# Kernel optimization log

Measured on AMD Instinct MI355X. Metric: run time of the kernel, lower is better.

The kernel has to match this reference:

```python
import jax, jax.numpy as jnp
import numpy as np

B, F, V, D = 16384, 26, 100000, 64
H1, H2 = 512, 256
IN_DIM = F * D + F * (F - 1) // 2  # 1664 + 325 = 1989
# upper-triangle (i<j) pair indices in row-major order == itertools.combinations order
IU, JU = np.triu_indices(F, k=1)


def setup_inputs() -> dict:
    key = jax.random.key(0)
    ks = jax.random.split(key, 9)
    idx = jax.random.randint(ks[0], (B, F), 0, V)
    tables = jax.random.normal(ks[1], (F, V, D), dtype=jnp.float32) * 0.01
    W1 = jax.random.normal(ks[2], (IN_DIM, H1), dtype=jnp.float32) * (IN_DIM ** -0.5)
    b1 = jnp.zeros((H1,), jnp.float32)
    W2 = jax.random.normal(ks[3], (H1, H2), dtype=jnp.float32) * (H1 ** -0.5)
    b2 = jnp.zeros((H2,), jnp.float32)
    W3 = jax.random.normal(ks[4], (H2, 1), dtype=jnp.float32) * (H2 ** -0.5)
    b3 = jnp.zeros((1,), jnp.float32)
    return {"idx": idx, "tables": tables, "W1": W1, "b1": b1,
            "W2": W2, "b2": b2, "W3": W3, "b3": b3}


def reference(idx, tables, W1, b1, W2, b2, W3, b3):
    # embedding lookup: tables[f, idx[b, f]] -> [B, F, D]
    emb = tables[jnp.arange(F)[None, :], idx]
    # fused dot-interaction: batched Gram matrix + triangular gather
    gram = jnp.einsum('bfd,bgd->bfg', emb, emb)  # [B, F, F]
    inter = gram[:, IU, JU]                      # [B, F*(F-1)/2]
    joint = jnp.concatenate([emb.reshape(B, F * D), inter], axis=1)
    h = jax.nn.relu(joint @ W1 + b1)
    h = jax.nn.relu(h @ W2 + b2)
    return (h @ W3 + b3).squeeze(-1)  # [B] logits
```

## Files before the change

kernel.cpp:

```cpp
#include <hip/hip_runtime.h>

#define B_SZ   16384
#define F_N    26
#define V_N    100000
#define D_N    64
#define H1_N   512
#define H2_N   256
#define IN_DIM 1989
#define KPAD   2048

typedef _Float16 half8_t __attribute__((ext_vector_type(8)));
typedef _Float16 half4_t __attribute__((ext_vector_type(4)));
typedef float    floatx4 __attribute__((ext_vector_type(4)));

#define MFMA16(a, b, c) __builtin_amdgcn_mfma_f32_16x16x32_f16((a), (b), (c), 0, 0, 0)

__device__ __forceinline__ void load_lds16(const void* g, void* l) {
    __builtin_amdgcn_global_load_lds(
        (const __attribute__((address_space(1))) unsigned int*)g,
        (__attribute__((address_space(3))) unsigned int*)l,
        16, 0, 0);
}

__global__ __launch_bounds__(256) void prep_w(const float* __restrict__ W,
                                              _Float16* __restrict__ WT,
                                              int K, int N, int Kpad) {
    int t = blockIdx.x * 256 + threadIdx.x;
    if (t >= N * Kpad) return;
    int k = t / N;
    int n = t - k * N;
    WT[(size_t)n * Kpad + k] = (k < K) ? (_Float16)W[(size_t)k * N + n] : (_Float16)0.f;
}

#define EMB_STRIDE 72
#define EMB_PER_SAMPLE (32 * EMB_STRIDE)

__global__ __launch_bounds__(256) void gather_interact(
        const int* __restrict__ idx,
        const float* __restrict__ tables,
        _Float16* __restrict__ joint) {
    __shared__ __align__(16) _Float16 embh[4 * EMB_PER_SAMPLE];
    __shared__ int sidx[4 * F_N];
    const int tid = threadIdx.x;
    const int b0  = blockIdx.x * 4;

    if (tid < 4 * F_N) sidx[tid] = idx[(size_t)b0 * F_N + tid];

    for (int z = tid; z < 4 * 6 * 16; z += 256) {
        int s = z / 96, rem = z % 96;
        int f = F_N + rem / 16, d4 = (rem % 16) * 4;
        half4_t zz; zz[0] = 0; zz[1] = 0; zz[2] = 0; zz[3] = 0;
        *(half4_t*)(embh + s * EMB_PER_SAMPLE + f * EMB_STRIDE + d4) = zz;
    }
    __syncthreads();

    float4 v[7];
    #pragma unroll
    for (int i = 0; i < 7; ++i) {
        int c = tid + i * 256;
        if (c < 4 * F_N * 16) {
            int s = c / 416, rem = c - s * 416;
            int f = rem >> 4, d4 = (rem & 15) * 4;
            v[i] = *(const float4*)(tables +
                     ((size_t)f * V_N + sidx[s * F_N + f]) * D_N + d4);
        }
    }
    #pragma unroll
    for (int i = 0; i < 7; ++i) {
        int c = tid + i * 256;
        if (c < 4 * F_N * 16) {
            int s = c / 416, rem = c - s * 416;
            int f = rem >> 4, d4 = (rem & 15) * 4;
            half4_t h;
            h[0] = (_Float16)v[i].x; h[1] = (_Float16)v[i].y;
            h[2] = (_Float16)v[i].z; h[3] = (_Float16)v[i].w;
            *(half4_t*)(embh + s * EMB_PER_SAMPLE + f * EMB_STRIDE + d4) = h;
            *(half4_t*)(joint + (size_t)(b0 + s) * KPAD + f * D_N + d4) = h;
        }
    }
    for (int q = tid; q < 4 * (KPAD - IN_DIM); q += 256) {
        int s = q / (KPAD - IN_DIM), p = q % (KPAD - IN_DIM);
        joint[(size_t)(b0 + s) * KPAD + IN_DIM + p] = (_Float16)0.f;
    }
    __syncthreads();

    const int wave = tid >> 6, lane = tid & 63;
    const _Float16* eb = embh + wave * EMB_PER_SAMPLE;
    const int fr = lane & 15;
    const int fk = (lane >> 4) * 8;
    floatx4 a00 = {0.f, 0.f, 0.f, 0.f};
    floatx4 a01 = {0.f, 0.f, 0.f, 0.f};
    floatx4 a11 = {0.f, 0.f, 0.f, 0.f};
    #pragma unroll
    for (int k0 = 0; k0 < 64; k0 += 32) {
        half8_t f0 = *(const half8_t*)(eb + fr * EMB_STRIDE + k0 + fk);
        half8_t f1 = *(const half8_t*)(eb + (16 + fr) * EMB_STRIDE + k0 + fk);
        a00 = MFMA16(f0, f0, a00);
        a01 = MFMA16(f0, f1, a01);
        a11 = MFMA16(f1, f1, a11);
    }
    _Float16* jrow = joint + (size_t)(b0 + wave) * KPAD + F_N * D_N;
    #pragma unroll
    for (int r = 0; r < 4; ++r) {
        int mb = (lane >> 4) * 4 + r;
        {
            int m = mb, n = fr;
            if (m < n) jrow[(m * (51 - m)) / 2 + n - m - 1] = (_Float16)a00[r];
        }
        {
            int m = mb, n = 16 + fr;
            if (n < F_N) jrow[(m * (51 - m)) / 2 + n - m - 1] = (_Float16)a01[r];
        }
        {
            int m = 16 + mb, n = 16 + fr;
            if (m < n && n < F_N) jrow[(m * (51 - m)) / 2 + n - m - 1] = (_Float16)a11[r];
        }
    }
}

__global__ __launch_bounds__(256) void gemm_bt(
        const _Float16* __restrict__ A, int lda,
        const _Float16* __restrict__ Bt, int ldb,
        const float* __restrict__ bias,
        _Float16* __restrict__ C, int ldc,
        int K, int nblocks) {
    __shared__ __align__(16) _Float16 As[128 * 32];
    __shared__ __align__(16) _Float16 Bs[128 * 32];
    const int tid  = threadIdx.x;
    const int wave = tid >> 6;
    const int lane = tid & 63;
    int bid = blockIdx.x;
    if ((gridDim.x & 7) == 0) {
        const int cpx = gridDim.x >> 3;
        bid = (bid & 7) * cpx + (bid >> 3);
    }
    const int bm = bid / nblocks;
    const int bn = bid % nblocks;
    const int m0 = bm * 128, n0 = bn * 128;

    const int c0 = tid, c1 = tid + 256;
    const _Float16* ag0 = A  + (size_t)(m0 + (c0 >> 2)) * lda + (c0 & 3) * 8;
    const _Float16* ag1 = A  + (size_t)(m0 + (c1 >> 2)) * lda + (c1 & 3) * 8;
    const _Float16* bg0 = Bt + (size_t)(n0 + (c0 >> 2)) * ldb + (c0 & 3) * 8;
    const _Float16* bg1 = Bt + (size_t)(n0 + (c1 >> 2)) * ldb + (c1 & 3) * 8;
    char* asd0 = (char*)As + wave * 1024;
    char* asd1 = (char*)As + 4096 + wave * 1024;
    char* bsd0 = (char*)Bs + wave * 1024;
    char* bsd1 = (char*)Bs + 4096 + wave * 1024;

    floatx4 acc[4][4];
    #pragma unroll
    for (int i = 0; i < 4; ++i)
        #pragma unroll
        for (int j = 0; j < 4; ++j) acc[i][j] = (floatx4){0.f, 0.f, 0.f, 0.f};

    const int wm = (wave >> 1) * 64;
    const int wn = (wave & 1) * 64;
    const int fr = lane & 15;
    const int fk = (lane >> 4) * 8;

    for (int k0 = 0; k0 < K; k0 += 32) {
        load_lds16(ag0 + k0, asd0);
        load_lds16(ag1 + k0, asd1);
        load_lds16(bg0 + k0, bsd0);
        load_lds16(bg1 + k0, bsd1);
        __syncthreads();
        half8_t af[4], bf[4];
        #pragma unroll
        for (int i = 0; i < 4; ++i)
            af[i] = *(const half8_t*)(As + (wm + i * 16 + fr) * 32 + fk);
        #pragma unroll
        for (int j = 0; j < 4; ++j)
            bf[j] = *(const half8_t*)(Bs + (wn + j * 16 + fr) * 32 + fk);
        #pragma unroll
        for (int i = 0; i < 4; ++i)
            #pragma unroll
            for (int j = 0; j < 4; ++j)
                acc[i][j] = MFMA16(af[i], bf[j], acc[i][j]);
        __syncthreads();
    }

    const int colb = n0 + wn + fr;
    const int rowb = m0 + wm + (lane >> 4) * 4;
    #pragma unroll
    for (int j = 0; j < 4; ++j) {
        const int c = colb + j * 16;
        const float bv = bias[c];
        #pragma unroll
        for (int i = 0; i < 4; ++i)
            #pragma unroll
            for (int r = 0; r < 4; ++r) {
                float v = acc[i][j][r] + bv;
                v = fmaxf(v, 0.f);
                C[(size_t)(rowb + i * 16 + r) * ldc + c] = (_Float16)v;
            }
    }
}

__global__ __launch_bounds__(512) void fused_tail(
        const _Float16* __restrict__ h1, const _Float16* __restrict__ W2T,
        const float* __restrict__ b2, const float* __restrict__ W3,
        const float* __restrict__ b3, float* __restrict__ out) {
    __shared__ __align__(16) _Float16 As[128 * 32];
    __shared__ __align__(16) _Float16 Bs[256 * 32];
    __shared__ float red[4][128];
    const int tid  = threadIdx.x;
    const int wave = tid >> 6;
    const int lane = tid & 63;
    const int m0 = blockIdx.x * 128;

    const int ca = tid, cb0 = tid, cb1 = tid + 512;
    const _Float16* ag  = h1  + (size_t)(m0 + (ca >> 2)) * H1_N + (ca & 3) * 8;
    const _Float16* bg0 = W2T + (size_t)(cb0 >> 2) * H1_N + (cb0 & 3) * 8;
    const _Float16* bg1 = W2T + (size_t)(cb1 >> 2) * H1_N + (cb1 & 3) * 8;
    char* asd  = (char*)As + wave * 1024;
    char* bsd0 = (char*)Bs + wave * 1024;
    char* bsd1 = (char*)Bs + 8192 + wave * 1024;

    floatx4 acc[4][4];
    #pragma unroll
    for (int i = 0; i < 4; ++i)
        #pragma unroll
        for (int j = 0; j < 4; ++j) acc[i][j] = (floatx4){0.f, 0.f, 0.f, 0.f};

    const int wm = (wave >> 2) * 64;
    const int wn = (wave & 3) * 64;
    const int fr = lane & 15;
    const int fk = (lane >> 4) * 8;

    for (int k0 = 0; k0 < H1_N; k0 += 32) {
        load_lds16(ag  + k0, asd);
        load_lds16(bg0 + k0, bsd0);
        load_lds16(bg1 + k0, bsd1);
        __syncthreads();
        half8_t af[4], bf[4];
        #pragma unroll
        for (int i = 0; i < 4; ++i)
            af[i] = *(const half8_t*)(As + (wm + i * 16 + fr) * 32 + fk);
        #pragma unroll
        for (int j = 0; j < 4; ++j)
            bf[j] = *(const half8_t*)(Bs + (wn + j * 16 + fr) * 32 + fk);
        #pragma unroll
        for (int i = 0; i < 4; ++i)
            #pragma unroll
            for (int j = 0; j < 4; ++j)
                acc[i][j] = MFMA16(af[i], bf[j], acc[i][j]);
        __syncthreads();
    }

    float b2v[4], w3v[4];
    #pragma unroll
    for (int j = 0; j < 4; ++j) {
        const int c = wn + j * 16 + fr;
        b2v[j] = b2[c];
        w3v[j] = W3[c];
    }
    #pragma unroll
    for (int i = 0; i < 4; ++i)
        #pragma unroll
        for (int r = 0; r < 4; ++r) {
            float p = 0.f;
            #pragma unroll
            for (int j = 0; j < 4; ++j) {
                float h = acc[i][j][r] + b2v[j];
                h = fmaxf(h, 0.f);
                p += h * w3v[j];
            }
            p += __shfl_xor(p, 1, 16);
            p += __shfl_xor(p, 2, 16);
            p += __shfl_xor(p, 4, 16);
            p += __shfl_xor(p, 8, 16);
            if (fr == 0)
                red[wave & 3][wm + i * 16 + (lane >> 4) * 4 + r] = p;
        }
    __syncthreads();
    if (tid < 128) {
        float s = red[0][tid] + red[1][tid] + red[2][tid] + red[3][tid] + b3[0];
        out[m0 + tid] = s;
    }
}

extern "C" void kernel_launch(void* const* d_in, const int* in_sizes, int n_in,
                              void* d_out, int out_size, void* d_ws, size_t ws_size,
                              hipStream_t stream) {
    const int*   idx    = (const int*)d_in[0];
    const float* tables = (const float*)d_in[1];
    const float* W1     = (const float*)d_in[2];
    const float* b1     = (const float*)d_in[3];
    const float* W2     = (const float*)d_in[4];
    const float* b2     = (const float*)d_in[5];
    const float* W3     = (const float*)d_in[6];
    const float* b3     = (const float*)d_in[7];
    float* out = (float*)d_out;

    char* ws = (char*)d_ws;
    _Float16* joint = (_Float16*)(ws);
    _Float16* W1T   = (_Float16*)(ws + 67108864);
    _Float16* h1    = (_Float16*)(ws + 69206016);
    _Float16* W2T   = (_Float16*)(ws + 85983232);

    prep_w<<<(H1_N * KPAD + 255) / 256, 256, 0, stream>>>(W1, W1T, IN_DIM, H1_N, KPAD);
    prep_w<<<(H2_N * H1_N + 255) / 256, 256, 0, stream>>>(W2, W2T, H1_N, H2_N, H1_N);
    gather_interact<<<B_SZ / 4, 256, 0, stream>>>(idx, tables, joint);
    gemm_bt<<<(B_SZ / 128) * (H1_N / 128), 256, 0, stream>>>(
        joint, KPAD, W1T, KPAD, b1, h1, H1_N, KPAD, H1_N / 128);
    fused_tail<<<B_SZ / 128, 512, 0, stream>>>(h1, W2T, b2, W3, b3, out);
}
```

Baseline: 829.4 us.

## Double-buffer LDS in GEMM kernels and shrink fused tail tile to 64 rows

Both the first-layer GEMM and the fused tail GEMM now double-buffer their LDS tiles, so the asynchronous global-to-LDS loads for the next K slice are issued before the MFMAs on the current slice. This overlaps memory latency with compute and cuts one barrier per iteration. The fused tail also moves from 128-row, 512-thread blocks to 64-row, 256-thread blocks, doubling the grid to 256 blocks so all CUs are filled. In exchange, LDS use per block doubles, which may lower occupancy, and the full W2 tile is reloaded by twice as many blocks.

Result: no change. 824.8 us (-0.6%).

```diff
diff --git a/kernel.cpp b/kernel.cpp
--- a/kernel.cpp
+++ b/kernel.cpp
@@ -124,8 +124,8 @@
         const float* __restrict__ bias,
         _Float16* __restrict__ C, int ldc,
         int K, int nblocks) {
-    __shared__ __align__(16) _Float16 As[128 * 32];
-    __shared__ __align__(16) _Float16 Bs[128 * 32];
+    __shared__ __align__(16) _Float16 As[2][128 * 32];
+    __shared__ __align__(16) _Float16 Bs[2][128 * 32];
     const int tid  = threadIdx.x;
     const int wave = tid >> 6;
     const int lane = tid & 63;
@@ -143,10 +143,6 @@
     const _Float16* ag1 = A  + (size_t)(m0 + (c1 >> 2)) * lda + (c1 & 3) * 8;
     const _Float16* bg0 = Bt + (size_t)(n0 + (c0 >> 2)) * ldb + (c0 & 3) * 8;
     const _Float16* bg1 = Bt + (size_t)(n0 + (c1 >> 2)) * ldb + (c1 & 3) * 8;
-    char* asd0 = (char*)As + wave * 1024;
-    char* asd1 = (char*)As + 4096 + wave * 1024;
-    char* bsd0 = (char*)Bs + wave * 1024;
-    char* bsd1 = (char*)Bs + 4096 + wave * 1024;
 
     floatx4 acc[4][4];
     #pragma unroll
@@ -159,26 +155,41 @@
     const int fr = lane & 15;
     const int fk = (lane >> 4) * 8;
 
-    for (int k0 = 0; k0 < K; k0 += 32) {
-        load_lds16(ag0 + k0, asd0);
-        load_lds16(ag1 + k0, asd1);
-        load_lds16(bg0 + k0, bsd0);
-        load_lds16(bg1 + k0, bsd1);
-        __syncthreads();
+    auto stage = [&](int buf, int k0) {
+        char* ab = (char*)As + buf * 8192;
+        char* bb = (char*)Bs + buf * 8192;
+        load_lds16(ag0 + k0, ab + wave * 1024);
+        load_lds16(ag1 + k0, ab + 4096 + wave * 1024);
+        load_lds16(bg0 + k0, bb + wave * 1024);
+        load_lds16(bg1 + k0, bb + 4096 + wave * 1024);
+    };
+    auto compute = [&](int buf) {
+        const _Float16* as = &As[buf][0];
+        const _Float16* bs = &Bs[buf][0];
         half8_t af[4], bf[4];
         #pragma unroll
         for (int i = 0; i < 4; ++i)
-            af[i] = *(const half8_t*)(As + (wm + i * 16 + fr) * 32 + fk);
+            af[i] = *(const half8_t*)(as + (wm + i * 16 + fr) * 32 + fk);
         #pragma unroll
         for (int j = 0; j < 4; ++j)
-            bf[j] = *(const half8_t*)(Bs + (wn + j * 16 + fr) * 32 + fk);
+            bf[j] = *(const half8_t*)(bs + (wn + j * 16 + fr) * 32 + fk);
         #pragma unroll
         for (int i = 0; i < 4; ++i)
             #pragma unroll
             for (int j = 0; j < 4; ++j)
                 acc[i][j] = MFMA16(af[i], bf[j], acc[i][j]);
+    };
+
+    stage(0, 0);
+    __syncthreads();
+    int cur = 0;
+    for (int k0 = 32; k0 < K; k0 += 32) {
+        stage(cur ^ 1, k0);
+        compute(cur);
         __syncthreads();
-    }
+        cur ^= 1;
+    }
+    compute(cur);
 
     const int colb = n0 + wn + fr;
     const int rowb = m0 + wm + (lane >> 4) * 4;
@@ -197,25 +208,20 @@
     }
 }
 
-__global__ __launch_bounds__(512) void fused_tail(
+__global__ __launch_bounds__(256) void fused_tail(
         const _Float16* __restrict__ h1, const _Float16* __restrict__ W2T,
         const float* __restrict__ b2, const float* __restrict__ W3,
         const float* __restrict__ b3, float* __restrict__ out) {
-    __shared__ __align__(16) _Float16 As[128 * 32];
-    __shared__ __align__(16) _Float16 Bs[256 * 32];
-    __shared__ float red[4][128];
+    __shared__ __align__(16) _Float16 As[2][64 * 32];
+    __shared__ __align__(16) _Float16 Bs[2][256 * 32];
+    __shared__ float red[4][64];
     const int tid  = threadIdx.x;
     const int wave = tid >> 6;
     const int lane = tid & 63;
-    const int m0 = blockIdx.x * 128;
-
-    const int ca = tid, cb0 = tid, cb1 = tid + 512;
-    const _Float16* ag  = h1  + (size_t)(m0 + (ca >> 2)) * H1_N + (ca & 3) * 8;
-    const _Float16* bg0 = W2T + (size_t)(cb0 >> 2) * H1_N + (cb0 & 3) * 8;
-    const _Float16* bg1 = W2T + (size_t)(cb1 >> 2) * H1_N + (cb1 & 3) * 8;
-    char* asd  = (char*)As + wave * 1024;
-    char* bsd0 = (char*)Bs + wave * 1024;
-    char* bsd1 = (char*)Bs + 8192 + wave * 1024;
+    const int m0 = blockIdx.x * 64;
+
+    const _Float16* ag  = h1  + (size_t)(m0 + (tid >> 2)) * H1_N + (tid & 3) * 8;
+    const _Float16* bg0 = W2T + (size_t)(tid >> 2) * H1_N + (tid & 3) * 8;
 
     floatx4 acc[4][4];
     #pragma unroll
@@ -223,30 +229,46 @@
         #pragma unroll
         for (int j = 0; j < 4; ++j) acc[i][j] = (floatx4){0.f, 0.f, 0.f, 0.f};
 
-    const int wm = (wave >> 2) * 64;
-    const int wn = (wave & 3) * 64;
+    const int wn = wave * 64;
     const int fr = lane & 15;
     const int fk = (lane >> 4) * 8;
 
-    for (int k0 = 0; k0 < H1_N; k0 += 32) {
-        load_lds16(ag  + k0, asd);
-        load_lds16(bg0 + k0, bsd0);
-        load_lds16(bg1 + k0, bsd1);
-        __syncthreads();
+    auto stage = [&](int buf, int k0) {
+        char* ab = (char*)As + buf * 4096;
+        char* bb = (char*)Bs + buf * 16384;
+        load_lds16(ag + k0, ab + wave * 1024);
+        #pragma unroll
+        for (int i = 0; i < 4; ++i)
+            load_lds16(bg0 + (size_t)i * 64 * H1_N + k0,
+                       bb + i * 4096 + wave * 1024);
+    };
+    auto compute = [&](int buf) {
+        const _Float16* as = &As[buf][0];
+        const _Float16* bs = &Bs[buf][0];
         half8_t af[4], bf[4];
         #pragma unroll
         for (int i = 0; i < 4; ++i)
-            af[i] = *(const half8_t*)(As + (wm + i * 16 + fr) * 32 + fk);
+            af[i] = *(const half8_t*)(as + (i * 16 + fr) * 32 + fk);
         #pragma unroll
         for (int j = 0; j < 4; ++j)
-            bf[j] = *(const half8_t*)(Bs + (wn + j * 16 + fr) * 32 + fk);
+            bf[j] = *(const half8_t*)(bs + (wn + j * 16 + fr) * 32 + fk);
         #pragma unroll
         for (int i = 0; i < 4; ++i)
             #pragma unroll
             for (int j = 0; j < 4; ++j)
                 acc[i][j] = MFMA16(af[i], bf[j], acc[i][j]);
+    };
+
+    stage(0, 0);
+    __syncthreads();
+    int cur = 0;
+    for (int k0 = 32; k0 < H1_N; k0 += 32) {
+        stage(cur ^ 1, k0);
+        compute(cur);
         __syncthreads();
-    }
+        cur ^= 1;
+    }
+    compute(cur);
 
     float b2v[4], w3v[4];
     #pragma unroll
@@ -271,10 +293,10 @@
             p += __shfl_xor(p, 4, 16);
             p += __shfl_xor(p, 8, 16);
             if (fr == 0)
-                red[wave & 3][wm + i * 16 + (lane >> 4) * 4 + r] = p;
-        }
-    __syncthreads();
-    if (tid < 128) {
+                red[wave][i * 16 + (lane >> 4) * 4 + r] = p;
+        }
+    __syncthreads();
+    if (tid < 64) {
         float s = red[0][tid] + red[1][tid] + red[2][tid] + red[3][tid] + b3[0];
         out[m0 + tid] = s;
     }
@@ -304,5 +326,5 @@
     gather_interact<<<B_SZ / 4, 256, 0, stream>>>(idx, tables, joint);
     gemm_bt<<<(B_SZ / 128) * (H1_N / 128), 256, 0, stream>>>(
         joint, KPAD, W1T, KPAD, b1, h1, H1_N, KPAD, H1_N / 128);
-    fused_tail<<<B_SZ / 128, 512, 0, stream>>>(h1, W2T, b2, W3, b3, out);
-}
+    fused_tail<<<B_SZ / 64, 256, 0, stream>>>(h1, W2T, b2, W3, b3, out);
+}
```
